# Kernel optimization log

Hardware: AMD Instinct MI355X
Metric: run time of the kernel (lower is better)

The kernel has to match this reference:

```python
import jax, jax.numpy as jnp
import numpy as np

PATCH = 7
STACK = 16
TUBE = 2
IMG = 84
EMBED = 1024
GH = IMG // PATCH   # 12
GW = IMG // PATCH   # 12
GD = STACK // TUBE  # 8
PF = 1 * PATCH * PATCH  # per-frame patch feature (C*p*p) = 49


def _sincos_1d(dim, pos):
    # pos: [N] -> [N, dim]
    omega = 1.0 / (10000.0 ** (np.arange(dim // 2, dtype=np.float64) / (dim / 2.0)))
    out = pos[:, None].astype(np.float64) * omega[None, :]
    return np.concatenate([np.sin(out), np.cos(out)], axis=1)


def get_3d_sincos_pos_embed(grid_h, grid_w, grid_depth, embed_dim):
    # standard video sincos split: 1/4 temporal, 3/4 spatial (half h, half w)
    dim_t = embed_dim // 4
    dim_s = embed_dim - dim_t
    emb_t = _sincos_1d(dim_t, np.arange(grid_depth))            # [D, dim_t]
    emb_h = _sincos_1d(dim_s // 2, np.arange(grid_h))           # [gh, dim_s/2]
    emb_w = _sincos_1d(dim_s - dim_s // 2, np.arange(grid_w))   # [gw, ...]
    # spatial tokens row-major (h major, w minor), matching unfold ordering
    emb_hw = np.concatenate(
        [np.repeat(emb_h, grid_w, axis=0), np.tile(emb_w, (grid_h, 1))], axis=1
    )  # [gh*gw, dim_s]
    ns = grid_h * grid_w
    # token order: depth major, spatial minor (matches D*Ns reshape in forward)
    pe = np.concatenate(
        [np.repeat(emb_t, ns, axis=0), np.tile(emb_hw, (grid_depth, 1))], axis=1
    )  # [D*Ns, embed_dim]
    return pe.astype(np.float32)


def setup_inputs() -> dict:
    key = jax.random.key(0)
    k1, k2, k3 = jax.random.split(key, 3)
    B = 64
    video = jax.random.normal(k1, (B, STACK, 1, IMG, IMG), dtype=jnp.float32)
    tubelet_in = TUBE * PF  # 98
    W = jax.random.normal(k2, (EMBED, tubelet_in), dtype=jnp.float32) * (tubelet_in ** -0.5)
    b = jax.random.normal(k3, (EMBED,), dtype=jnp.float32) * 0.02
    pos_embed = jnp.asarray(get_3d_sincos_pos_embed(GH, GW, GD, EMBED))[None]  # [1, N, E]
    return {"video": video, "W": W, "b": b, "pos_embed": pos_embed}


def reference(video, W, b, pos_embed):
    B, T, C, H, W_ = video.shape
    p = PATCH
    gh, gw = H // p, W_ // p
    ns = gh * gw
    # extract_tensor_patches (stride == window, no padding): pure reshape/transpose
    x = video.reshape(B * T, C, gh, p, gw, p)
    x = x.transpose(0, 2, 4, 1, 3, 5)                 # [BT, gh, gw, C, p, p]
    x = x.reshape(B, T, ns, C * p * p)                # [B, T, Ns, Pf]
    x = x.reshape(B, GD, TUBE, ns, C * p * p)
    x = x.transpose(0, 1, 3, 2, 4)                    # [B, D, Ns, Ts, Pf]
    tubelets = x.reshape(B, GD * ns, TUBE * C * p * p)  # [B, N, 98]
    tokens = jnp.einsum("bnk,ek->bne", tubelets, W) + b + pos_embed
    return tokens
```

## Files before the change

### kernel.cpp

```cpp
#include <hip/hip_runtime.h>
#include <hip/hip_bf16.h>
#include <stdint.h>


typedef __bf16 bf16_t;
typedef bf16_t bf16x8 __attribute__((ext_vector_type(8)));
typedef float f32x4 __attribute__((ext_vector_type(4)));

#define B_      64
#define N_TOK   1152
#define M_TOT   (B_ * N_TOK)
#define E_      1024
#define KP      128
#define K_REAL  98
#define BM      128
#define BN      128
#define MT_N    (M_TOT / BM)
#define NT_N    (E_ / BN)

__global__ void wconv_kernel(const float* __restrict__ W, bf16_t* __restrict__ Wb) {
    int idx = blockIdx.x * 256 + threadIdx.x;
    int k = idx & (KP - 1);
    int e = idx >> 7;
    float v = (k < K_REAL) ? W[e * K_REAL + k] : 0.f;
    Wb[e * KP + (k ^ ((e & 7) << 3))] = (bf16_t)v;
}

__global__ __launch_bounds__(256) void gemm_kernel(
    const float* __restrict__ video, const bf16_t* __restrict__ Wb,
    const float* __restrict__ bias, const float* __restrict__ pos,
    float* __restrict__ out) {
    __shared__ __align__(16) bf16_t As[BM * KP];
    __shared__ __align__(16) bf16_t Bs[BN * KP];

    const int tid  = threadIdx.x;
    const int wv   = tid >> 6;
    const int lane = tid & 63;

    const int bid = blockIdx.x;
    const int nt  = bid & 7;
    const int mt  = bid >> 3;
    const long m0 = (long)mt * BM;
    const int  n0 = nt * BN;
    const int  bb = mt / 9;
    const int  ntok_blk = (mt - bb * 9) * BM;

    {
        const char* gB = (const char*)(Wb + (long)n0 * KP);
        char* lB = (char*)Bs;
#pragma unroll
        for (int i = 0; i < 8; ++i) {
            int off = (wv * 8 + i) * 1024;
            __builtin_amdgcn_global_load_lds(
                (const __attribute__((address_space(1))) void*)(gB + off + lane * 16),
                (__attribute__((address_space(3))) void*)(lB + off), 16, 0, 0);
        }
    }

    {
        const float* vbase = video + (size_t)(bb * 16) * 7056;
#pragma unroll
        for (int it = 0; it < 8; ++it) {
            int gi    = it * 256 + tid;
            int m_loc = gi >> 4;
            int g     = gi & 15;
            int n  = ntok_blk + m_loc;
            int d  = n / 144, s = n - d * 144;
            int i  = s / 12,  jj = s - i * 12;
            const float* fbase = vbase + (size_t)(d * 2) * 7056 + (i * 7) * 84 + jj * 7;
            bf16_t vals[8];
#pragma unroll
            for (int u = 0; u < 8; ++u) {
                int k = g * 8 + u;
                float v = 0.f;
                if (k < K_REAL) {
                    int ts = (k >= 49) ? 1 : 0;
                    int f  = k - ts * 49;
                    int fy = f / 7, fx = f - fy * 7;
                    v = fbase[ts * 7056 + fy * 84 + fx];
                }
                vals[u] = (bf16_t)v;
            }
            int col = (g * 8) ^ ((m_loc & 7) << 3);
            *(bf16x8*)&As[m_loc * KP + col] = *(const bf16x8*)vals;
        }
    }
    __syncthreads();

    const int we = wv >> 1, wt = wv & 1;
    const int lr = lane & 15;
    const int lk = (lane >> 4) * 8;
    const int xsw = (lr & 7) << 3;

    f32x4 acc[4][4];
#pragma unroll
    for (int ei = 0; ei < 4; ++ei)
#pragma unroll
        for (int ti = 0; ti < 4; ++ti)
            acc[ei][ti] = (f32x4){0.f, 0.f, 0.f, 0.f};

#pragma unroll
    for (int kk = 0; kk < 4; ++kk) {
        bf16x8 a[4], b[4];
        const int col = (kk * 32 + lk) ^ xsw;
#pragma unroll
        for (int ei = 0; ei < 4; ++ei)
            a[ei] = *(const bf16x8*)&Bs[(we * 64 + ei * 16 + lr) * KP + col];
#pragma unroll
        for (int ti = 0; ti < 4; ++ti)
            b[ti] = *(const bf16x8*)&As[(wt * 64 + ti * 16 + lr) * KP + col];
#pragma unroll
        for (int ei = 0; ei < 4; ++ei)
#pragma unroll
            for (int ti = 0; ti < 4; ++ti)
                acc[ei][ti] = __builtin_amdgcn_mfma_f32_16x16x32_bf16(
                    a[ei], b[ti], acc[ei][ti], 0, 0, 0);
    }

    const int row4 = (lane >> 4) * 4;
#pragma unroll
    for (int ei = 0; ei < 4; ++ei) {
        const int e_base = n0 + we * 64 + ei * 16 + row4;
        const f32x4 bias4 = *(const f32x4*)&bias[e_base];
#pragma unroll
        for (int ti = 0; ti < 4; ++ti) {
            const int tok = wt * 64 + ti * 16 + lr;
            const f32x4 pos4 = *(const f32x4*)&pos[(ntok_blk + tok) * E_ + e_base];
            f32x4 vout = acc[ei][ti] + bias4 + pos4;
            __builtin_nontemporal_store(
                vout, (f32x4*)&out[(m0 + tok) * (long)E_ + e_base]);
        }
    }
}

extern "C" void kernel_launch(void* const* d_in, const int* in_sizes, int n_in,
                              void* d_out, int out_size, void* d_ws, size_t ws_size,
                              hipStream_t stream) {
    const float* video = (const float*)d_in[0];
    const float* W     = (const float*)d_in[1];
    const float* bias  = (const float*)d_in[2];
    const float* pos   = (const float*)d_in[3];
    float* out = (float*)d_out;

    bf16_t* W_ws = (bf16_t*)d_ws;

    wconv_kernel<<<(E_ * KP) / 256, 256, 0, stream>>>(W, W_ws);
    gemm_kernel<<<MT_N * NT_N, 256, 0, stream>>>(video, W_ws, bias, pos, out);
}
```

Measured before the change: 517.3 us.

## Keep weight fragments in registers and loop over token chunks without LDS

Replaces the LDS-staged single-tile GEMM with a persistent-style kernel. Each wave loads its weight MFMA fragments and bias into registers once, then loops over 8 token chunks, gathering video patches straight from global memory into MFMA operand registers. This drops shared memory, the barrier, and the repeated weight loads per tile, and skips padded K work in the last k-step. The cost is heavy register pressure under launch_bounds(256,2), uncoalesced per-lane gathers, and 8x fewer blocks, which reduces parallelism.

```diff
diff --git a/kernel.cpp b/kernel.cpp
--- a/kernel.cpp
+++ b/kernel.cpp
@@ -7,128 +7,118 @@
 typedef bf16_t bf16x8 __attribute__((ext_vector_type(8)));
 typedef float f32x4 __attribute__((ext_vector_type(4)));
 
-#define B_      64
-#define N_TOK   1152
-#define M_TOT   (B_ * N_TOK)
 #define E_      1024
 #define KP      128
 #define K_REAL  98
-#define BM      128
-#define BN      128
-#define MT_N    (M_TOT / BM)
-#define NT_N    (E_ / BN)
+#define N_TOK   1152
+#define M_TOT   73728
+#define CHUNK   128
+#define NCHUNK  (M_TOT / CHUNK)
+#define CPB     8
+#define MG_N    (NCHUNK / CPB)
+#define GRID    (MG_N * 8)
 
 __global__ void wconv_kernel(const float* __restrict__ W, bf16_t* __restrict__ Wb) {
     int idx = blockIdx.x * 256 + threadIdx.x;
     int k = idx & (KP - 1);
     int e = idx >> 7;
-    float v = (k < K_REAL) ? W[e * K_REAL + k] : 0.f;
-    Wb[e * KP + (k ^ ((e & 7) << 3))] = (bf16_t)v;
+    Wb[idx] = (bf16_t)((k < K_REAL) ? W[e * K_REAL + k] : 0.f);
 }
 
-__global__ __launch_bounds__(256) void gemm_kernel(
+__global__ __launch_bounds__(256, 2) void embed_kernel(
     const float* __restrict__ video, const bf16_t* __restrict__ Wb,
     const float* __restrict__ bias, const float* __restrict__ pos,
     float* __restrict__ out) {
-    __shared__ __align__(16) bf16_t As[BM * KP];
-    __shared__ __align__(16) bf16_t Bs[BN * KP];
-
     const int tid  = threadIdx.x;
     const int wv   = tid >> 6;
     const int lane = tid & 63;
+    const int we   = wv >> 1, wt = wv & 1;
+    const int lr   = lane & 15;
+    const int hi   = lane >> 4;
+    const int lk   = hi * 8;
 
     const int bid = blockIdx.x;
     const int nt  = bid & 7;
-    const int mt  = bid >> 3;
-    const long m0 = (long)mt * BM;
-    const int  n0 = nt * BN;
-    const int  bb = mt / 9;
-    const int  ntok_blk = (mt - bb * 9) * BM;
+    const int mg  = bid >> 3;
+    const int n0  = nt * 128 + we * 64;
 
-    {
-        const char* gB = (const char*)(Wb + (long)n0 * KP);
-        char* lB = (char*)Bs;
+    bf16x8 wfrag[4][4];
 #pragma unroll
-        for (int i = 0; i < 8; ++i) {
-            int off = (wv * 8 + i) * 1024;
-            __builtin_amdgcn_global_load_lds(
-                (const __attribute__((address_space(1))) void*)(gB + off + lane * 16),
-                (__attribute__((address_space(3))) void*)(lB + off), 16, 0, 0);
-        }
-    }
+    for (int ei = 0; ei < 4; ++ei)
+#pragma unroll
+        for (int kk = 0; kk < 4; ++kk)
+            wfrag[ei][kk] = *(const bf16x8*)&Wb[(n0 + ei * 16 + lr) * KP + kk * 32 + lk];
 
-    {
-        const float* vbase = video + (size_t)(bb * 16) * 7056;
+    f32x4 bias4[4];
 #pragma unroll
-        for (int it = 0; it < 8; ++it) {
-            int gi    = it * 256 + tid;
-            int m_loc = gi >> 4;
-            int g     = gi & 15;
-            int n  = ntok_blk + m_loc;
-            int d  = n / 144, s = n - d * 144;
-            int i  = s / 12,  jj = s - i * 12;
-            const float* fbase = vbase + (size_t)(d * 2) * 7056 + (i * 7) * 84 + jj * 7;
-            bf16_t vals[8];
+    for (int ei = 0; ei < 4; ++ei)
+        bias4[ei] = *(const f32x4*)&bias[n0 + ei * 16 + hi * 4];
+
+#pragma unroll 1
+    for (int j = 0; j < CPB; ++j) {
+        const int m0 = (mg * CPB + j) * CHUNK + wt * 64;
+
+        bf16x8 bfrag[4][4];
 #pragma unroll
-            for (int u = 0; u < 8; ++u) {
-                int k = g * 8 + u;
-                float v = 0.f;
-                if (k < K_REAL) {
+        for (int ti = 0; ti < 4; ++ti) {
+            const int m = m0 + ti * 16 + lr;
+            const int b = m / N_TOK;
+            const int n = m - b * N_TOK;
+            const int d = n / 144, s = n - d * 144;
+            const int iy = s / 12, jx = s - iy * 12;
+            const float* fb = video + (size_t)(b * 16 + d * 2) * 7056
+                              + iy * 7 * 84 + jx * 7;
+#pragma unroll
+            for (int kk = 0; kk < 3; ++kk) {
+                bf16_t tmp[8];
+#pragma unroll
+                for (int u = 0; u < 8; ++u) {
+                    int k  = kk * 32 + lk + u;
                     int ts = (k >= 49) ? 1 : 0;
                     int f  = k - ts * 49;
                     int fy = f / 7, fx = f - fy * 7;
-                    v = fbase[ts * 7056 + fy * 84 + fx];
+                    tmp[u] = (bf16_t)fb[ts * 7056 + fy * 84 + fx];
                 }
-                vals[u] = (bf16_t)v;
+                bfrag[ti][kk] = *(const bf16x8*)tmp;
             }
-            int col = (g * 8) ^ ((m_loc & 7) << 3);
-            *(bf16x8*)&As[m_loc * KP + col] = *(const bf16x8*)vals;
+            {
+                bf16_t tmp[8] = {bf16_t(0.f), bf16_t(0.f), bf16_t(0.f), bf16_t(0.f),
+                                 bf16_t(0.f), bf16_t(0.f), bf16_t(0.f), bf16_t(0.f)};
+                if (hi == 0) {
+                    tmp[0] = (bf16_t)fb[7565];
+                    tmp[1] = (bf16_t)fb[7566];
+                }
+                bfrag[ti][3] = *(const bf16x8*)tmp;
+            }
         }
-    }
-    __syncthreads();
 
-    const int we = wv >> 1, wt = wv & 1;
-    const int lr = lane & 15;
-    const int lk = (lane >> 4) * 8;
-    const int xsw = (lr & 7) << 3;
-
-    f32x4 acc[4][4];
-#pragma unroll
-    for (int ei = 0; ei < 4; ++ei)
-#pragma unroll
-        for (int ti = 0; ti < 4; ++ti)
-            acc[ei][ti] = (f32x4){0.f, 0.f, 0.f, 0.f};
-
-#pragma unroll
-    for (int kk = 0; kk < 4; ++kk) {
-        bf16x8 a[4], b[4];
-        const int col = (kk * 32 + lk) ^ xsw;
-#pragma unroll
-        for (int ei = 0; ei < 4; ++ei)
-            a[ei] = *(const bf16x8*)&Bs[(we * 64 + ei * 16 + lr) * KP + col];
-#pragma unroll
-        for (int ti = 0; ti < 4; ++ti)
-            b[ti] = *(const bf16x8*)&As[(wt * 64 + ti * 16 + lr) * KP + col];
+        f32x4 acc[4][4];
 #pragma unroll
         for (int ei = 0; ei < 4; ++ei)
 #pragma unroll
             for (int ti = 0; ti < 4; ++ti)
-                acc[ei][ti] = __builtin_amdgcn_mfma_f32_16x16x32_bf16(
-                    a[ei], b[ti], acc[ei][ti], 0, 0, 0);
-    }
+                acc[ei][ti] = (f32x4){0.f, 0.f, 0.f, 0.f};
+#pragma unroll
+        for (int kk = 0; kk < 4; ++kk)
+#pragma unroll
+            for (int ei = 0; ei < 4; ++ei)
+#pragma unroll
+                for (int ti = 0; ti < 4; ++ti)
+                    acc[ei][ti] = __builtin_amdgcn_mfma_f32_16x16x32_bf16(
+                        wfrag[ei][kk], bfrag[ti][kk], acc[ei][ti], 0, 0, 0);
 
-    const int row4 = (lane >> 4) * 4;
-#pragma unroll
-    for (int ei = 0; ei < 4; ++ei) {
-        const int e_base = n0 + we * 64 + ei * 16 + row4;
-        const f32x4 bias4 = *(const f32x4*)&bias[e_base];
 #pragma unroll
         for (int ti = 0; ti < 4; ++ti) {
-            const int tok = wt * 64 + ti * 16 + lr;
-            const f32x4 pos4 = *(const f32x4*)&pos[(ntok_blk + tok) * E_ + e_base];
-            f32x4 vout = acc[ei][ti] + bias4 + pos4;
-            __builtin_nontemporal_store(
-                vout, (f32x4*)&out[(m0 + tok) * (long)E_ + e_base]);
+            const int m    = m0 + ti * 16 + lr;
+            const int ntok = m % N_TOK;
+#pragma unroll
+            for (int ei = 0; ei < 4; ++ei) {
+                const int e_base = n0 + ei * 16 + hi * 4;
+                const f32x4 pos4 = *(const f32x4*)&pos[(size_t)ntok * E_ + e_base];
+                f32x4 vout = acc[ei][ti] + bias4[ei] + pos4;
+                __builtin_nontemporal_store(
+                    vout, (f32x4*)&out[(size_t)m * E_ + e_base]);
+            }
         }
     }
 }
@@ -145,5 +135,5 @@
     bf16_t* W_ws = (bf16_t*)d_ws;
 
     wconv_kernel<<<(E_ * KP) / 256, 256, 0, stream>>>(W, W_ws);
-    gemm_kernel<<<MT_N * NT_N, 256, 0, stream>>>(video, W_ws, bias, pos, out);
+    embed_kernel<<<GRID, 256, 0, stream>>>(video, W_ws, bias, pos, out);
 }
```

After: 498.7 us. 3.6% less time.
